# Kernel tuning notes

Measured on AMD Instinct MI355X. Metric: run time of the kernel, lower is better.

The kernel has to match this reference:

```python
import jax, jax.numpy as jnp
import numpy as np

B = 16        # graphs per batch
NPG = 4096    # nodes per graph
N = B * NPG
EPG = 32768   # edges per graph
E = B * EPG
F_NODE, F_EDGE, G, H, A = 8, 4, 16, 128, 10


def setup_inputs() -> dict:
    key = jax.random.key(0)
    ks = jax.random.split(key, 32)
    x = jax.random.normal(ks[0], (N, F_NODE), jnp.float32)
    # random intra-graph edges, offset into the batched node id space
    src = jax.random.randint(ks[1], (B, EPG), 0, NPG)
    dst = jax.random.randint(ks[2], (B, EPG), 0, NPG)
    off = (jnp.arange(B) * NPG)[:, None]
    edge_index = jnp.stack([(src + off).reshape(-1), (dst + off).reshape(-1)]).astype(jnp.int64)
    edge_attr = jax.random.normal(ks[3], (E, F_EDGE), jnp.float32)
    global_state = jax.random.normal(ks[4], (B, G), jnp.float32)
    current_pipe_nodes = jax.random.randint(ks[5], (B, 2), 0, NPG).astype(jnp.int64)

    def w(k, shape):
        fan_in = shape[0] if len(shape) > 1 else shape[0]
        return jax.random.normal(k, shape, jnp.float32) * (1.0 / np.sqrt(fan_in))

    return dict(
        x=x, edge_index=edge_index, edge_attr=edge_attr,
        global_state=global_state, current_pipe_nodes=current_pipe_nodes,
        W_l1=w(ks[6], (F_NODE, H)), W_r1=w(ks[7], (F_NODE, H)), W_e1=w(ks[8], (F_EDGE, H)),
        att1=w(ks[9], (H,)), b1=jnp.zeros((H,), jnp.float32),
        W_l2=w(ks[10], (H, H)), W_r2=w(ks[11], (H, H)), W_e2=w(ks[12], (F_EDGE, H)),
        att2=w(ks[13], (H,)), b2=jnp.zeros((H,), jnp.float32),
        W_c=w(ks[14], (H + 2 * H + G, 256)), b_c=jnp.zeros((256,), jnp.float32),
        W_a1=w(ks[15], (256, 128)), b_a1=jnp.zeros((128,), jnp.float32),
        W_a2=w(ks[16], (128, A)), b_a2=jnp.zeros((A,), jnp.float32),
        W_v1=w(ks[17], (256, 128)), b_v1=jnp.zeros((128,), jnp.float32),
        W_v2=w(ks[18], (128, 1)), b_v2=jnp.zeros((1,), jnp.float32),
    )


def add_self_loops(edge_index, edge_attr, n):
    # PyG default: add_self_loops=True, fill_value='mean' -> loop attr is the
    # mean of incoming edge_attr per node (zeros if none).
    dst = edge_index[1]
    deg = jax.ops.segment_sum(jnp.ones(dst.shape, jnp.float32), dst, num_segments=n)
    loop_attr = jax.ops.segment_sum(edge_attr, dst, num_segments=n) / jnp.maximum(deg, 1.0)[:, None]
    loops = jnp.tile(jnp.arange(n, dtype=edge_index.dtype)[None, :], (2, 1))
    ei = jnp.concatenate([edge_index, loops], axis=1)
    ea = jnp.concatenate([edge_attr, loop_attr], axis=0)
    return ei, ea


def gatv2(x, ei, ea, Wl, Wr, We, att, bias, n):
    # GATv2Conv (heads=1): score = att . leaky_relu(Wl x_j + Wr x_i + We e_ij)
    # message = alpha_ij * (Wl x_j); segment softmax over incoming edges of i.
    src, dst = ei[0], ei[1]
    xl = x @ Wl                                   # [N,H]
    xr = x @ Wr                                   # [N,H]
    m = xl[src] + xr[dst] + ea @ We               # [E,H]
    s = jax.nn.leaky_relu(m, 0.2) @ att           # [E]
    smax = jax.ops.segment_max(s, dst, num_segments=n)
    ealpha = jnp.exp(s - smax[dst])
    denom = jax.ops.segment_sum(ealpha, dst, num_segments=n)
    alpha = ealpha / denom[dst]
    out = jax.ops.segment_sum(alpha[:, None] * xl[src], dst, num_segments=n)
    return out + bias


def reference(x, edge_index, edge_attr, global_state, current_pipe_nodes,
              W_l1, W_r1, W_e1, att1, b1,
              W_l2, W_r2, W_e2, att2, b2,
              W_c, b_c, W_a1, b_a1, W_a2, b_a2, W_v1, b_v1, W_v2, b_v2):
    ei, ea = add_self_loops(edge_index, edge_attr, N)
    h = jax.nn.relu(gatv2(x, ei, ea, W_l1, W_r1, W_e1, att1, b1, N))
    h = gatv2(h, ei, ea, W_l2, W_r2, W_e2, att2, b2, N)
    # global_mean_pool: graphs are contiguous equal-size blocks
    graph_emb = h.reshape(B, NPG, H).mean(axis=1)                       # [B,H]
    abs_idx = current_pipe_nodes + (jnp.arange(B) * NPG)[:, None]       # [B,2]
    pipe_emb = h[abs_idx.reshape(-1)].reshape(B, 2 * H)                 # [B,2H]
    comb = jnp.concatenate([graph_emb, pipe_emb, global_state], axis=1)
    feat = jax.nn.relu(comb @ W_c + b_c)
    logits = jax.nn.relu(feat @ W_a1 + b_a1) @ W_a2 + b_a2              # [B,A]
    value = jax.nn.relu(feat @ W_v1 + b_v1) @ W_v2 + b_v2               # [B,1]
    return jnp.concatenate([logits, value], axis=1)                     # [B,A+1]
```

## Files before the change

kernel.cpp:

```cpp
#include <hip/hip_runtime.h>
#include <math.h>

#define NN   65536
#define NPG  4096
#define NB   16
#define NE   524288
#define EPG  32768
#define SB   8
#define NH   128
#define FN   8
#define FE   4
#define NG   16
#define NA   10
#define NFRAG 2048

typedef __attribute__((ext_vector_type(8))) short bf16x8;
typedef __attribute__((ext_vector_type(4))) float f32x4;

static __device__ __forceinline__ short bf16rne(float f) {
    unsigned u = __builtin_bit_cast(unsigned, f);
    u += 0x7FFFu + ((u >> 16) & 1u);
    return (short)(u >> 16);
}

__global__ void hist_lin1_kernel(const int* __restrict__ ei, int* __restrict__ subhist,
                                 const float* __restrict__ x,
                                 const float* __restrict__ Wl, const float* __restrict__ Wr,
                                 float* __restrict__ xl, float* __restrict__ xr) {
    int bid = blockIdx.x;
    if (bid < NB * SB) {
        __shared__ int hh[NPG];
        int g = bid >> 3, sb = bid & 7;
        int t = threadIdx.x;
        for (int i = t; i < NPG; i += 256) hh[i] = 0;
        __syncthreads();
        const int* dstp = ei + NE + g * EPG + sb * (EPG / SB);
        for (int i = t; i < EPG / SB; i += 256)
            atomicAdd(&hh[dstp[i] - g * NPG], 1);
        __syncthreads();
        int* out = subhist + (size_t)bid * NPG;
        for (int i = t; i < NPG; i += 256) out[i] = hh[i];
    } else {
        __shared__ float row[2][FN];
        int b2 = bid - NB * SB;
        int sub = threadIdx.x >> 7;
        int k = threadIdx.x & 127;
        int n = b2 * 2 + sub;
        if (k < FN) row[sub][k] = x[n * FN + k];
        __syncthreads();
        float al = 0.f, ar = 0.f;
#pragma unroll
        for (int j = 0; j < FN; ++j) {
            float v = row[sub][j];
            al += v * Wl[j * NH + k];
            ar += v * Wr[j * NH + k];
        }
        xl[n * NH + k] = al;
        xr[n * NH + k] = ar;
    }
}

__global__ __launch_bounds__(1024) void scan_kernel(
        const int* __restrict__ subhist, int* __restrict__ offs, int* __restrict__ cur2,
        const float* __restrict__ Wl2, const float* __restrict__ Wr2,
        bf16x8* __restrict__ wbf) {
    int g = blockIdx.x, t = threadIdx.x;
    if (g >= NB) {
        int sel = g - NB;
        const float* W = sel ? Wr2 : Wl2;
#pragma unroll
        for (int q = 0; q < 2; ++q) {
            int f = t * 2 + q;
            int lane = f & 63;
            int kgct = f >> 6;
            int kg = kgct & 3, ct = kgct >> 2;
            int kbase = kg * 32 + (lane >> 4) * 8;
            int c = ct * 16 + (lane & 15);
            bf16x8 v;
#pragma unroll
            for (int j = 0; j < 8; ++j)
                v[j] = bf16rne(W[(kbase + j) * NH + c]);
            wbf[sel * NFRAG + f] = v;
        }
        return;
    }
    __shared__ int psum[1024];
    int h[4][SB];
    int loc[4];
    int run = 0;
#pragma unroll
    for (int i = 0; i < 4; ++i) {
        int nl = t * 4 + i;
        int d = 0;
#pragma unroll
        for (int sb = 0; sb < SB; ++sb) {
            int v = subhist[((size_t)(g * SB + sb)) * NPG + nl];
            h[i][sb] = v;
            d += v;
        }
        loc[i] = run;
        run += d;
    }
    psum[t] = run;
    __syncthreads();
    for (int s = 1; s < 1024; s <<= 1) {
        int add = (t >= s) ? psum[t - s] : 0;
        __syncthreads();
        psum[t] += add;
        __syncthreads();
    }
    int prefix = (t == 0) ? 0 : psum[t - 1];
    int ebase = g * EPG;
#pragma unroll
    for (int i = 0; i < 4; ++i) {
        int nl = t * 4 + i;
        int off = ebase + prefix + loc[i];
        offs[g * NPG + nl] = off;
        int running = off;
#pragma unroll
        for (int sb = 0; sb < SB; ++sb) {
            cur2[((size_t)(g * SB + sb)) * NPG + nl] = running;
            running += h[i][sb];
        }
    }
    if (g == NB - 1 && t == 0) offs[NN] = NE;
}

__global__ __launch_bounds__(1024) void csr_fill_kernel(
        const int* __restrict__ ei, const int* __restrict__ cur2, int2* __restrict__ csr) {
    __shared__ int cur[NPG];
    int bid = blockIdx.x;
    int g = bid >> 3, sb = bid & 7;
    int t = threadIdx.x;
    const int* base = cur2 + (size_t)bid * NPG;
    for (int i = t; i < NPG; i += 1024) cur[i] = base[i];
    __syncthreads();
    int e0 = g * EPG + sb * (EPG / SB);
#pragma unroll
    for (int i = 0; i < (EPG / SB) / 1024; ++i) {
        int e = e0 + i * 1024 + t;
        int dst = ei[NE + e];
        int src = ei[e];
        int pos = atomicAdd(&cur[dst - g * NPG], 1);
        csr[pos] = make_int2(src, e);
    }
}

__global__ __launch_bounds__(256) void gat_gather_kernel(
        const float4* __restrict__ xl, const float4* __restrict__ xr,
        const float4* __restrict__ ea,
        const int2* __restrict__ csr, const int* __restrict__ offs,
        const float* __restrict__ We, const float* __restrict__ att,
        const float* __restrict__ bias, float* __restrict__ out,
        unsigned short* __restrict__ hbf_out,
        float4* __restrict__ lattr_w, const float4* __restrict__ lattr_r,
        float4* __restrict__ gpart, int do_relu) {
    __shared__ float4 red[8][32];
    int grp = threadIdx.x >> 5;
    int lane = threadIdx.x & 31;
    int bid = blockIdx.x;
    int xcd = bid & 7, slot = bid >> 3;
    int g = xcd + ((slot >> 9) << 3);
    int blk = slot & 511;
    int node = g * NPG + blk * 8 + grp;

    float4 xr4 = xr[node * 32 + lane];
    float4 att4 = ((const float4*)att)[lane];
    const float4* We4 = (const float4*)We;
    float4 we0 = We4[lane];
    float4 we1 = We4[32 + lane];
    float4 we2 = We4[64 + lane];
    float4 we3 = We4[96 + lane];

    int beg = offs[node], end = offs[node + 1];
    float l = 0.f;
    float4 acc = make_float4(0.f, 0.f, 0.f, 0.f);
    float4 easum = make_float4(0.f, 0.f, 0.f, 0.f);
    bool have_lattr = (lattr_r != nullptr);
    if (beg < end) {
        int last = end - 1;
        int2 se0 = csr[beg];
        int p1 = (beg + 1 <= last) ? beg + 1 : last;
        int2 se1 = csr[p1];
        float4 xl0 = xl[se0.x * 32 + lane];
        float4 a0 = ea[se0.y];
        for (int p = beg; p < end; ++p) {
            int p2 = (p + 2 <= last) ? p + 2 : last;
            int2 se2 = csr[p2];
            float4 xl1 = xl[se1.x * 32 + lane];
            float4 a1 = ea[se1.y];
            if (!have_lattr) {
                easum.x += a0.x; easum.y += a0.y; easum.z += a0.z; easum.w += a0.w;
            }
            float tx = xl0.x + xr4.x + a0.x * we0.x + a0.y * we1.x + a0.z * we2.x + a0.w * we3.x;
            float ty = xl0.y + xr4.y + a0.x * we0.y + a0.y * we1.y + a0.z * we2.y + a0.w * we3.y;
            float tz = xl0.z + xr4.z + a0.x * we0.z + a0.y * we1.z + a0.z * we2.z + a0.w * we3.z;
            float tw = xl0.w + xr4.w + a0.x * we0.w + a0.y * we1.w + a0.z * we2.w + a0.w * we3.w;
            tx = tx > 0.f ? tx : 0.2f * tx;
            ty = ty > 0.f ? ty : 0.2f * ty;
            tz = tz > 0.f ? tz : 0.2f * tz;
            tw = tw > 0.f ? tw : 0.2f * tw;
            float s = tx * att4.x + ty * att4.y + tz * att4.z + tw * att4.w;
#pragma unroll
            for (int o = 16; o >= 1; o >>= 1) s += __shfl_xor(s, o);
            float w = __expf(s);
            l += w;
            acc.x += w * xl0.x;
            acc.y += w * xl0.y;
            acc.z += w * xl0.z;
            acc.w += w * xl0.w;
            se1 = se2; xl0 = xl1; a0 = a1;
        }
    }
    {
        float ax, ay, az, aw;
        if (have_lattr) {
            float4 la = lattr_r[node];
            ax = la.x; ay = la.y; az = la.z; aw = la.w;
        } else {
            int deg = end - beg;
            float invd = 1.0f / (float)(deg > 0 ? deg : 1);
            ax = easum.x * invd; ay = easum.y * invd;
            az = easum.z * invd; aw = easum.w * invd;
            if (lane == 0) lattr_w[node] = make_float4(ax, ay, az, aw);
        }
        float4 xl4 = xl[node * 32 + lane];
        float tx = xl4.x + xr4.x + ax * we0.x + ay * we1.x + az * we2.x + aw * we3.x;
        float ty = xl4.y + xr4.y + ax * we0.y + ay * we1.y + az * we2.y + aw * we3.y;
        float tz = xl4.z + xr4.z + ax * we0.z + ay * we1.z + az * we2.z + aw * we3.z;
        float tw = xl4.w + xr4.w + ax * we0.w + ay * we1.w + az * we2.w + aw * we3.w;
        tx = tx > 0.f ? tx : 0.2f * tx;
        ty = ty > 0.f ? ty : 0.2f * ty;
        tz = tz > 0.f ? tz : 0.2f * tz;
        tw = tw > 0.f ? tw : 0.2f * tw;
        float s = tx * att4.x + ty * att4.y + tz * att4.z + tw * att4.w;
#pragma unroll
        for (int o = 16; o >= 1; o >>= 1) s += __shfl_xor(s, o);
        float w = __expf(s);
        l += w;
        acc.x += w * xl4.x;
        acc.y += w * xl4.y;
        acc.z += w * xl4.z;
        acc.w += w * xl4.w;
    }
    float inv = 1.0f / l;
    float4 b4 = ((const float4*)bias)[lane];
    float4 o4;
    o4.x = acc.x * inv + b4.x;
    o4.y = acc.y * inv + b4.y;
    o4.z = acc.z * inv + b4.z;
    o4.w = acc.w * inv + b4.w;
    if (do_relu) {
        o4.x = fmaxf(o4.x, 0.f); o4.y = fmaxf(o4.y, 0.f);
        o4.z = fmaxf(o4.z, 0.f); o4.w = fmaxf(o4.w, 0.f);
    }
    if (hbf_out != nullptr) {
        int rt = node >> 4, m = node & 15;
        int kg = lane >> 3, qd = (lane & 7) >> 1, j0 = (lane & 1) * 4;
        ushort4 v;
        v.x = (unsigned short)bf16rne(o4.x);
        v.y = (unsigned short)bf16rne(o4.y);
        v.z = (unsigned short)bf16rne(o4.z);
        v.w = (unsigned short)bf16rne(o4.w);
        *(ushort4*)&hbf_out[(size_t)(((rt * 4 + kg) * 64 + qd * 16 + m)) * 8 + j0] = v;
    } else {
        ((float4*)out)[node * 32 + lane] = o4;
    }

    if (gpart != nullptr) {
        red[grp][lane] = o4;
        __syncthreads();
        if (grp < 4) {
            float4 o = red[grp + 4][lane];
            red[grp][lane] = make_float4(red[grp][lane].x + o.x, red[grp][lane].y + o.y,
                                         red[grp][lane].z + o.z, red[grp][lane].w + o.w);
        }
        __syncthreads();
        if (grp < 2) {
            float4 o = red[grp + 2][lane];
            red[grp][lane] = make_float4(red[grp][lane].x + o.x, red[grp][lane].y + o.y,
                                         red[grp][lane].z + o.z, red[grp][lane].w + o.w);
        }
        __syncthreads();
        if (grp == 0) {
            float4 a = red[0][lane], b = red[1][lane];
            gpart[(g * 512 + blk) * 32 + lane] =
                make_float4(a.x + b.x, a.y + b.y, a.z + b.z, a.w + b.w);
        }
    }
}

__global__ __launch_bounds__(256) void lin2_mfma_kernel(
        const bf16x8* __restrict__ hbf, const bf16x8* __restrict__ wbf,
        float* __restrict__ xl, float* __restrict__ xr) {
    const bf16x8* Bf = wbf + (size_t)blockIdx.y * NFRAG;
    float* C = blockIdx.y ? xr : xl;
    int t = threadIdx.x;
    int wv = t >> 6, lane = t & 63;
    int rt = blockIdx.x * 4 + wv;
    int row0 = rt * 16;
    int m = lane & 15, qd = lane >> 4;
    bf16x8 afrag[4];
#pragma unroll
    for (int kg = 0; kg < 4; ++kg)
        afrag[kg] = hbf[(size_t)(rt * 4 + kg) * 64 + lane];
#pragma unroll
    for (int ct = 0; ct < 8; ++ct) {
        f32x4 acc = {0.f, 0.f, 0.f, 0.f};
#pragma unroll
        for (int kg = 0; kg < 4; ++kg) {
            bf16x8 b = Bf[((ct << 2) | kg) * 64 + lane];
            acc = __builtin_amdgcn_mfma_f32_16x16x32_bf16(afrag[kg], b, acc, 0, 0, 0);
        }
        int col = ct * 16 + m;
#pragma unroll
        for (int r = 0; r < 4; ++r)
            C[(size_t)(row0 + qd * 4 + r) * NH + col] = acc[r];
    }
}

__global__ void head_kernel(const float* __restrict__ gpart, const float* __restrict__ h,
                            const float* __restrict__ gstate, const int* __restrict__ cpn,
                            const float* __restrict__ Wc, const float* __restrict__ bc,
                            const float* __restrict__ Wa1, const float* __restrict__ ba1,
                            const float* __restrict__ Wa2, const float* __restrict__ ba2,
                            const float* __restrict__ Wv1, const float* __restrict__ bv1,
                            const float* __restrict__ Wv2, const float* __restrict__ bv2,
                            float* __restrict__ out) {
    int b = blockIdx.x, t = threadIdx.x;
    __shared__ float comb[400];
    __shared__ float feat[256];
    __shared__ float hid[256];
    int n0 = cpn[b * 2 + 0] + b * NPG;
    int n1 = cpn[b * 2 + 1] + b * NPG;
    if (t < 128) {
        float s0 = 0.f, s1 = 0.f, s2 = 0.f, s3 = 0.f;
        const float* gp = gpart + (size_t)b * 512 * NH + t;
        for (int c = 0; c < 512; c += 4) {
            s0 += gp[(c + 0) * NH];
            s1 += gp[(c + 1) * NH];
            s2 += gp[(c + 2) * NH];
            s3 += gp[(c + 3) * NH];
        }
        comb[t] = (s0 + s1 + s2 + s3) * (1.0f / NPG);
        comb[128 + t] = h[n0 * NH + t];
    } else {
        int tt = t - 128;
        comb[256 + tt] = h[n1 * NH + tt];
        if (tt < NG) comb[384 + tt] = gstate[b * NG + tt];
    }
    __syncthreads();
    float acc = bc[t];
    for (int j = 0; j < 400; ++j) acc += comb[j] * Wc[j * 256 + t];
    feat[t] = fmaxf(acc, 0.f);
    __syncthreads();
    if (t < 128) {
        float a2 = ba1[t];
        for (int j = 0; j < 256; ++j) a2 += feat[j] * Wa1[j * NH + t];
        hid[t] = fmaxf(a2, 0.f);
    } else {
        int tt = t - 128;
        float a2 = bv1[tt];
        for (int j = 0; j < 256; ++j) a2 += feat[j] * Wv1[j * NH + tt];
        hid[128 + tt] = fmaxf(a2, 0.f);
    }
    __syncthreads();
    if (t < NA) {
        float a2 = ba2[t];
        for (int j = 0; j < NH; ++j) a2 += hid[j] * Wa2[j * NA + t];
        out[b * 11 + t] = a2;
    } else if (t == NA) {
        float a2 = bv2[0];
        for (int j = 0; j < NH; ++j) a2 += hid[128 + j] * Wv2[j];
        out[b * 11 + 10] = a2;
    }
}

extern "C" void kernel_launch(void* const* d_in, const int* in_sizes, int n_in,
                              void* d_out, int out_size, void* d_ws, size_t ws_size,
                              hipStream_t stream) {
    const float* x      = (const float*)d_in[0];
    const int*   ei     = (const int*)d_in[1];
    const float* ea     = (const float*)d_in[2];
    const float* gstate = (const float*)d_in[3];
    const int*   cpn    = (const int*)d_in[4];
    const float* Wl1 = (const float*)d_in[5];
    const float* Wr1 = (const float*)d_in[6];
    const float* We1 = (const float*)d_in[7];
    const float* att1= (const float*)d_in[8];
    const float* b1  = (const float*)d_in[9];
    const float* Wl2 = (const float*)d_in[10];
    const float* Wr2 = (const float*)d_in[11];
    const float* We2 = (const float*)d_in[12];
    const float* att2= (const float*)d_in[13];
    const float* b2  = (const float*)d_in[14];
    const float* Wc  = (const float*)d_in[15];
    const float* bc  = (const float*)d_in[16];
    const float* Wa1 = (const float*)d_in[17];
    const float* ba1 = (const float*)d_in[18];
    const float* Wa2 = (const float*)d_in[19];
    const float* ba2 = (const float*)d_in[20];
    const float* Wv1 = (const float*)d_in[21];
    const float* bv1 = (const float*)d_in[22];
    const float* Wv2 = (const float*)d_in[23];
    const float* bv2 = (const float*)d_in[24];

    char* ws = (char*)d_ws;
    size_t o = 0;
    float* xl     = (float*)(ws + o); o += (size_t)NN * NH * 4;
    float* xr     = (float*)(ws + o); o += (size_t)NN * NH * 4;
    float* h      = (float*)(ws + o); o += (size_t)NN * NH * 4;
    unsigned short* hbf = (unsigned short*)(ws + o); o += (size_t)NN * NH * 2;
    float* lattr  = (float*)(ws + o); o += (size_t)NN * 16;
    float* gpart  = (float*)(ws + o); o += (size_t)NB * 512 * NH * 4;
    int*   offs   = (int*)(ws + o);   o += (((size_t)(NN + 1) * 4 + 255) & ~(size_t)255);
    int*   subhist= (int*)(ws + o);   o += (size_t)NB * SB * NPG * 4;
    int*   cur2   = (int*)(ws + o);   o += (size_t)NB * SB * NPG * 4;
    int2*  csr    = (int2*)(ws + o);  o += (size_t)NE * 8;
    bf16x8* wbf   = (bf16x8*)(ws + o); o += (size_t)2 * NFRAG * 16;
    (void)o; (void)ws_size; (void)in_sizes; (void)n_in; (void)out_size;

    hist_lin1_kernel<<<NB * SB + NN / 2, 256, 0, stream>>>(ei, subhist, x, Wl1, Wr1, xl, xr);
    scan_kernel<<<NB + 2, 1024, 0, stream>>>(subhist, offs, cur2, Wl2, Wr2, wbf);
    csr_fill_kernel<<<NB * SB, 1024, 0, stream>>>(ei, cur2, csr);
    gat_gather_kernel<<<NN / 8, 256, 0, stream>>>((const float4*)xl, (const float4*)xr,
        (const float4*)ea, csr, offs, We1, att1, b1, nullptr, hbf,
        (float4*)lattr, nullptr, nullptr, 1);
    lin2_mfma_kernel<<<dim3(NN / 64, 2), 256, 0, stream>>>((const bf16x8*)hbf, wbf, xl, xr);
    gat_gather_kernel<<<NN / 8, 256, 0, stream>>>((const float4*)xl, (const float4*)xr,
        (const float4*)ea, csr, offs, We2, att2, b2, h, nullptr,
        nullptr, (const float4*)lattr, (float4*)gpart, 0);
    head_kernel<<<NB, 256, 0, stream>>>(gpart, h, gstate, cpn, Wc, bc, Wa1, ba1, Wa2, ba2,
                                        Wv1, bv1, Wv2, bv2, (float*)d_out);
}
```

Baseline: 315.1 us.

## Replace per-block graph partials with atomic sums and widen head kernel

The second gather kernel now accumulates per-graph mean-pool sums straight into a small global buffer with float atomics, instead of writing 512 partial rows per graph. The buffer is zeroed in the scan kernel. The head kernel no longer serially reduces the partials, and it runs with 1024 threads that split each dense-layer dot product into four K-chunks combined through shared memory. This targets the serial latency of the 16-block head kernel, at the cost of atomic contention (512 blocks per graph hitting the same 128 addresses) and non-deterministic summation order.

New measurement: 344.8 us. 1.09x slower.

```diff
diff --git a/kernel.cpp b/kernel.cpp
--- a/kernel.cpp
+++ b/kernel.cpp
@@ -63,10 +63,12 @@
 __global__ __launch_bounds__(1024) void scan_kernel(
         const int* __restrict__ subhist, int* __restrict__ offs, int* __restrict__ cur2,
         const float* __restrict__ Wl2, const float* __restrict__ Wr2,
-        bf16x8* __restrict__ wbf) {
+        bf16x8* __restrict__ wbf, float* __restrict__ gsum) {
     int g = blockIdx.x, t = threadIdx.x;
     if (g >= NB) {
         int sel = g - NB;
+        if (sel == 0 && t < 512)
+            ((float4*)gsum)[t] = make_float4(0.f, 0.f, 0.f, 0.f);
         const float* W = sel ? Wr2 : Wl2;
 #pragma unroll
         for (int q = 0; q < 2; ++q) {
@@ -154,7 +156,7 @@
         const float* __restrict__ bias, float* __restrict__ out,
         unsigned short* __restrict__ hbf_out,
         float4* __restrict__ lattr_w, const float4* __restrict__ lattr_r,
-        float4* __restrict__ gpart, int do_relu) {
+        float* __restrict__ gsum, int do_relu) {
     __shared__ float4 red[8][32];
     int grp = threadIdx.x >> 5;
     int lane = threadIdx.x & 31;
@@ -267,7 +269,7 @@
         ((float4*)out)[node * 32 + lane] = o4;
     }
 
-    if (gpart != nullptr) {
+    if (gsum != nullptr) {
         red[grp][lane] = o4;
         __syncthreads();
         if (grp < 4) {
@@ -284,8 +286,11 @@
         __syncthreads();
         if (grp == 0) {
             float4 a = red[0][lane], b = red[1][lane];
-            gpart[(g * 512 + blk) * 32 + lane] =
-                make_float4(a.x + b.x, a.y + b.y, a.z + b.z, a.w + b.w);
+            float* gs = gsum + (size_t)g * NH + lane * 4;
+            atomicAdd(gs + 0, a.x + b.x);
+            atomicAdd(gs + 1, a.y + b.y);
+            atomicAdd(gs + 2, a.z + b.z);
+            atomicAdd(gs + 3, a.w + b.w);
         }
     }
 }
@@ -319,50 +324,51 @@
     }
 }
 
-__global__ void head_kernel(const float* __restrict__ gpart, const float* __restrict__ h,
-                            const float* __restrict__ gstate, const int* __restrict__ cpn,
-                            const float* __restrict__ Wc, const float* __restrict__ bc,
-                            const float* __restrict__ Wa1, const float* __restrict__ ba1,
-                            const float* __restrict__ Wa2, const float* __restrict__ ba2,
-                            const float* __restrict__ Wv1, const float* __restrict__ bv1,
-                            const float* __restrict__ Wv2, const float* __restrict__ bv2,
-                            float* __restrict__ out) {
+__global__ __launch_bounds__(1024) void head_kernel(
+        const float* __restrict__ gsum, const float* __restrict__ h,
+        const float* __restrict__ gstate, const int* __restrict__ cpn,
+        const float* __restrict__ Wc, const float* __restrict__ bc,
+        const float* __restrict__ Wa1, const float* __restrict__ ba1,
+        const float* __restrict__ Wa2, const float* __restrict__ ba2,
+        const float* __restrict__ Wv1, const float* __restrict__ bv1,
+        const float* __restrict__ Wv2, const float* __restrict__ bv2,
+        float* __restrict__ out) {
     int b = blockIdx.x, t = threadIdx.x;
     __shared__ float comb[400];
+    __shared__ float part[4][256];
     __shared__ float feat[256];
     __shared__ float hid[256];
     int n0 = cpn[b * 2 + 0] + b * NPG;
     int n1 = cpn[b * 2 + 1] + b * NPG;
-    if (t < 128) {
-        float s0 = 0.f, s1 = 0.f, s2 = 0.f, s3 = 0.f;
-        const float* gp = gpart + (size_t)b * 512 * NH + t;
-        for (int c = 0; c < 512; c += 4) {
-            s0 += gp[(c + 0) * NH];
-            s1 += gp[(c + 1) * NH];
-            s2 += gp[(c + 2) * NH];
-            s3 += gp[(c + 3) * NH];
-        }
-        comb[t] = (s0 + s1 + s2 + s3) * (1.0f / NPG);
-        comb[128 + t] = h[n0 * NH + t];
-    } else {
-        int tt = t - 128;
-        comb[256 + tt] = h[n1 * NH + tt];
-        if (tt < NG) comb[384 + tt] = gstate[b * NG + tt];
-    }
-    __syncthreads();
-    float acc = bc[t];
-    for (int j = 0; j < 400; ++j) acc += comb[j] * Wc[j * 256 + t];
-    feat[t] = fmaxf(acc, 0.f);
-    __syncthreads();
-    if (t < 128) {
-        float a2 = ba1[t];
-        for (int j = 0; j < 256; ++j) a2 += feat[j] * Wa1[j * NH + t];
-        hid[t] = fmaxf(a2, 0.f);
-    } else {
-        int tt = t - 128;
-        float a2 = bv1[tt];
-        for (int j = 0; j < 256; ++j) a2 += feat[j] * Wv1[j * NH + tt];
-        hid[128 + tt] = fmaxf(a2, 0.f);
+    if (t < 128) comb[t] = gsum[b * NH + t] * (1.0f / NPG);
+    else if (t < 256) comb[t] = h[(size_t)n0 * NH + (t - 128)];
+    else if (t < 384) comb[t] = h[(size_t)n1 * NH + (t - 256)];
+    else if (t < 400) comb[t] = gstate[b * NG + (t - 384)];
+    __syncthreads();
+    {
+        int col = t & 255, p = t >> 8;
+        float a = 0.f;
+        int j0 = p * 100;
+        for (int j = j0; j < j0 + 100; ++j) a += comb[j] * Wc[j * 256 + col];
+        part[p][col] = a;
+    }
+    __syncthreads();
+    if (t < 256)
+        feat[t] = fmaxf(bc[t] + part[0][t] + part[1][t] + part[2][t] + part[3][t], 0.f);
+    __syncthreads();
+    {
+        int col = t & 255, p = t >> 8;
+        const float* W = (col < 128) ? Wa1 : Wv1;
+        int cc = col & 127;
+        float a = 0.f;
+        int j0 = p * 64;
+        for (int j = j0; j < j0 + 64; ++j) a += feat[j] * W[j * 128 + cc];
+        part[p][col] = a;
+    }
+    __syncthreads();
+    if (t < 256) {
+        float bias = (t < 128) ? ba1[t] : bv1[t - 128];
+        hid[t] = fmaxf(bias + part[0][t] + part[1][t] + part[2][t] + part[3][t], 0.f);
     }
     __syncthreads();
     if (t < NA) {
@@ -412,7 +418,7 @@
     float* h      = (float*)(ws + o); o += (size_t)NN * NH * 4;
     unsigned short* hbf = (unsigned short*)(ws + o); o += (size_t)NN * NH * 2;
     float* lattr  = (float*)(ws + o); o += (size_t)NN * 16;
-    float* gpart  = (float*)(ws + o); o += (size_t)NB * 512 * NH * 4;
+    float* gsum   = (float*)(ws + o); o += (size_t)NB * NH * 4;
     int*   offs   = (int*)(ws + o);   o += (((size_t)(NN + 1) * 4 + 255) & ~(size_t)255);
     int*   subhist= (int*)(ws + o);   o += (size_t)NB * SB * NPG * 4;
     int*   cur2   = (int*)(ws + o);   o += (size_t)NB * SB * NPG * 4;
@@ -421,7 +427,7 @@
     (void)o; (void)ws_size; (void)in_sizes; (void)n_in; (void)out_size;
 
     hist_lin1_kernel<<<NB * SB + NN / 2, 256, 0, stream>>>(ei, subhist, x, Wl1, Wr1, xl, xr);
-    scan_kernel<<<NB + 2, 1024, 0, stream>>>(subhist, offs, cur2, Wl2, Wr2, wbf);
+    scan_kernel<<<NB + 2, 1024, 0, stream>>>(subhist, offs, cur2, Wl2, Wr2, wbf, gsum);
     csr_fill_kernel<<<NB * SB, 1024, 0, stream>>>(ei, cur2, csr);
     gat_gather_kernel<<<NN / 8, 256, 0, stream>>>((const float4*)xl, (const float4*)xr,
         (const float4*)ea, csr, offs, We1, att1, b1, nullptr, hbf,
@@ -429,7 +435,7 @@
     lin2_mfma_kernel<<<dim3(NN / 64, 2), 256, 0, stream>>>((const bf16x8*)hbf, wbf, xl, xr);
     gat_gather_kernel<<<NN / 8, 256, 0, stream>>>((const float4*)xl, (const float4*)xr,
         (const float4*)ea, csr, offs, We2, att2, b2, h, nullptr,
-        nullptr, (const float4*)lattr, (float4*)gpart, 0);
-    head_kernel<<<NB, 256, 0, stream>>>(gpart, h, gstate, cpn, Wc, bc, Wa1, ba1, Wa2, ba2,
-                                        Wv1, bv1, Wv2, bv2, (float*)d_out);
-}
+        nullptr, (const float4*)lattr, gsum, 0);
+    head_kernel<<<NB, 1024, 0, stream>>>(gsum, h, gstate, cpn, Wc, bc, Wa1, ba1, Wa2, ba2,
+                                         Wv1, bv1, Wv2, bv2, (float*)d_out);
+}
```
